# Kernel optimization log

Hardware: AMD Instinct MI355X
Metric: run time of the kernel (lower is better)

The kernel has to match this reference:

```python
import jax, jax.numpy as jnp
import numpy as np

B, N, E = 64, 128, 262144
HID, NRBF, NBLK = 128, 64, 4
RCUT = 6.0
GAMMA = 10.0 / (RCUT * RCUT)


def setup_inputs() -> dict:
    key = jax.random.key(0)
    ks = jax.random.split(key, 20)
    s_rbf = 1.0 / np.sqrt(NRBF)
    s_hid = 1.0 / np.sqrt(HID)
    return {
        "Z": jax.random.randint(ks[0], (B, N), 0, 100),
        "pos": jax.random.normal(ks[1], (B, N, 3), dtype=jnp.float32) * 3.0,
        "edge_index": jax.random.randint(ks[2], (2, E), 0, B * N),
        "embed_w": jax.random.normal(ks[3], (100, HID), dtype=jnp.float32) * 0.02,
        "edge_w1": jax.random.normal(ks[4], (NBLK, NRBF, HID), dtype=jnp.float32) * s_rbf,
        "edge_b1": jnp.zeros((NBLK, HID), dtype=jnp.float32),
        "edge_w2": jax.random.normal(ks[5], (NBLK, HID, HID), dtype=jnp.float32) * s_hid,
        "edge_b2": jnp.zeros((NBLK, HID), dtype=jnp.float32),
        "lin_in_w": jax.random.normal(ks[6], (NBLK, HID, HID), dtype=jnp.float32) * s_hid,
        "node_w1": jax.random.normal(ks[7], (NBLK, HID, HID), dtype=jnp.float32) * s_hid,
        "node_b1": jnp.zeros((NBLK, HID), dtype=jnp.float32),
        "node_w2": jax.random.normal(ks[8], (NBLK, HID, HID), dtype=jnp.float32) * s_hid,
        "node_b2": jnp.zeros((NBLK, HID), dtype=jnp.float32),
        "ln_g": jnp.ones((NBLK, HID), dtype=jnp.float32),
        "ln_b": jnp.zeros((NBLK, HID), dtype=jnp.float32),
        "ro_w1": jax.random.normal(ks[9], (HID, HID // 2), dtype=jnp.float32) * s_hid,
        "ro_b1": jnp.zeros((HID // 2,), dtype=jnp.float32),
        "ro_w2": jax.random.normal(ks[10], (HID // 2, 1), dtype=jnp.float32) * (1.0 / np.sqrt(HID // 2)),
        "ro_b2": jnp.zeros((1,), dtype=jnp.float32),
    }


def _layernorm(x, g, b, eps=1e-5):
    mu = x.mean(-1, keepdims=True)
    var = ((x - mu) ** 2).mean(-1, keepdims=True)
    return (x - mu) / jnp.sqrt(var + eps) * g + b


def reference(Z, pos, edge_index, embed_w, edge_w1, edge_b1, edge_w2, edge_b2,
              lin_in_w, node_w1, node_b1, node_w2, node_b2, ln_g, ln_b,
              ro_w1, ro_b1, ro_w2, ro_b2):
    Zf = Z.reshape(-1)               # [B*N]
    pf = pos.reshape(-1, 3)          # [B*N, 3]
    src, dst = edge_index[0], edge_index[1]

    h = embed_w[Zf]                  # [B*N, H]

    # edge RBF features
    d = jnp.linalg.norm(pf[src] - pf[dst], axis=-1)      # [E]
    d = jnp.minimum(d, RCUT)
    centers = jnp.linspace(0.0, RCUT, NRBF)
    rbf = jnp.exp(-GAMMA * (d[:, None] - centers) ** 2)  # [E, NRBF]

    for i in range(NBLK):
        # CFConv: edge filter MLP on rbf
        w = jax.nn.silu(rbf @ edge_w1[i] + edge_b1[i]) @ edge_w2[i] + edge_b2[i]  # [E,H]
        m = w * (h[src] @ lin_in_w[i])                                            # [E,H]
        agg = jnp.zeros_like(h).at[dst].add(m)                                    # scatter-add [B*N,H]
        out = jax.nn.silu(agg @ node_w1[i] + node_b1[i]) @ node_w2[i] + node_b2[i]
        h = _layernorm(h + out, ln_g[i], ln_b[i])

    # readout: SiLU -> Linear -> SiLU -> Linear
    x = jax.nn.silu(h) @ ro_w1 + ro_b1
    e_atom = (jax.nn.silu(x) @ ro_w2 + ro_b2)[:, 0]      # [B*N]
    return e_atom.reshape(B, N).sum(axis=-1)             # per-graph energies [B]
```

## Files before the change

kernel.cpp:

```cpp
#include <hip/hip_runtime.h>

#define BN 8192
#define EE 262144
#define HIDD 128
#define NRBF 64
#define NBLK 4
#define TLUT 1024
#define CAP 128
#define MROWS 32
#define RCUTF 6.0f
#define GAMMAF (10.0f / 36.0f)

typedef unsigned short u16;
typedef __attribute__((ext_vector_type(8))) short short8x;
typedef __attribute__((ext_vector_type(4))) float f32x4;

__device__ __forceinline__ float silu_f(float v) {
    return v / (1.0f + __expf(-v));
}
__device__ __forceinline__ float bf2f(u16 u) {
    return __uint_as_float(((unsigned)u) << 16);
}
__device__ __forceinline__ u16 f2bf(float f) {
    unsigned u = __float_as_uint(f);
    unsigned r = u + 0x7FFFu + ((u >> 16) & 1u);
    return (u16)(r >> 16);
}

__global__ void k_prep(const float* __restrict__ liw, const float* __restrict__ nw1,
                       const float* __restrict__ nw2, const float* __restrict__ ro1,
                       u16* __restrict__ liwT, u16* __restrict__ nw1T,
                       u16* __restrict__ nw2T, u16* __restrict__ ro1T,
                       int* __restrict__ cnt, float* __restrict__ out, int out_n) {
    int id0 = blockIdx.x * 256 + threadIdx.x;
    for (int id = id0; id < 12 * 16384; id += 65536) {
        int which = id >> 14;
        int r = id & 16383;
        int n = r >> 7, k = r & 127;
        const float* src = which < 4 ? liw : (which < 8 ? nw1 : nw2);
        u16* dst = which < 4 ? liwT : (which < 8 ? nw1T : nw2T);
        int b = which & 3;
        dst[b * 16384 + n * 128 + k] = f2bf(src[(size_t)b * 16384 + k * 128 + n]);
    }
    if (id0 < 8192) {
        cnt[id0] = 0;
        int n = id0 >> 7, k = id0 & 127;
        ro1T[n * 128 + k] = f2bf(ro1[k * 64 + n]);
        if (id0 < out_n) out[id0] = 0.0f;
    }
}

__global__ void k_edges(const int* __restrict__ ei, const float* __restrict__ pos,
                        int* __restrict__ cnt, int2* __restrict__ meta) {
    int e = blockIdx.x * 256 + threadIdx.x;
    int s = ei[e];
    int d = ei[EE + e];
    float dx = pos[s * 3 + 0] - pos[d * 3 + 0];
    float dy = pos[s * 3 + 1] - pos[d * 3 + 1];
    float dz = pos[s * 3 + 2] - pos[d * 3 + 2];
    float dist = fminf(sqrtf(dx * dx + dy * dy + dz * dz), RCUTF);
    float f = dist * ((TLUT - 1) / RCUTF);
    int i0 = (int)f;
    i0 = i0 > TLUT - 2 ? TLUT - 2 : i0;
    float fr = f - (float)i0;
    int y = (i0 << 16) | (int)(fr * 65535.0f);
    int p = atomicAdd(&cnt[d], 1);
    if (p < CAP) meta[d * CAP + p] = make_int2(s, y);
}

#define GEMM_INNER(ACC, AROW0, K)                                              \
    {                                                                          \
        float4 wv = *(float4*)&Ws[K][c0];                                      \
        float a0 = AROW0[0], a1 = AROW0[1], a2 = AROW0[2], a3 = AROW0[3];      \
        ACC[0][0] += a0 * wv.x; ACC[0][1] += a0 * wv.y;                        \
        ACC[0][2] += a0 * wv.z; ACC[0][3] += a0 * wv.w;                        \
        ACC[1][0] += a1 * wv.x; ACC[1][1] += a1 * wv.y;                        \
        ACC[1][2] += a1 * wv.z; ACC[1][3] += a1 * wv.w;                        \
        ACC[2][0] += a2 * wv.x; ACC[2][1] += a2 * wv.y;                        \
        ACC[2][2] += a2 * wv.z; ACC[2][3] += a2 * wv.w;                        \
        ACC[3][0] += a3 * wv.x; ACC[3][1] += a3 * wv.y;                        \
        ACC[3][2] += a3 * wv.z; ACC[3][3] += a3 * wv.w;                        \
    }

__global__ __launch_bounds__(256) void k_lutall(const float* __restrict__ W1a,
                                                const float* __restrict__ b1a,
                                                const float* __restrict__ W2a,
                                                const float* __restrict__ b2a,
                                                u16* __restrict__ lutall) {
    __shared__ float As[32][33];
    __shared__ float Ws[32][128];
    __shared__ float T[32][128];
    int blk = blockIdx.x >> 5;
    int r0 = (blockIdx.x & 31) * 32;
    const float* W1 = W1a + (size_t)blk * NRBF * HIDD;
    const float* b1 = b1a + blk * HIDD;
    const float* W2 = W2a + (size_t)blk * HIDD * HIDD;
    const float* b2 = b2a + blk * HIDD;
    u16* lutp = lutall + (size_t)blk * TLUT * 256;
    int tid = threadIdx.x;
    int tx = tid & 31, ty = tid >> 5;
    int c0 = tx * 4, rr = ty * 4;
    float acc[4][4] = {};
    for (int kc = 0; kc < NRBF; kc += 32) {
        int lr = tid >> 3, lc = (tid & 7) * 4;
        float dt = (r0 + lr) * (RCUTF / (TLUT - 1));
#pragma unroll
        for (int j = 0; j < 4; ++j) {
            float c = (kc + lc + j) * (RCUTF / 63.0f);
            float u = dt - c;
            As[lr][lc + j] = __expf(-GAMMAF * u * u);
        }
#pragma unroll
        for (int j = 0; j < 4; ++j) {
            int idx = tid + j * 256;
            int wr = idx >> 5, wc = (idx & 31) * 4;
            *(float4*)&Ws[wr][wc] = *(const float4*)&W1[(size_t)(kc + wr) * HIDD + wc];
        }
        __syncthreads();
#pragma unroll 8
        for (int k = 0; k < 32; ++k) {
            float ar[4] = {As[rr][k], As[rr + 1][k], As[rr + 2][k], As[rr + 3][k]};
            GEMM_INNER(acc, ar, k)
        }
        __syncthreads();
    }
#pragma unroll
    for (int i = 0; i < 4; ++i)
#pragma unroll
        for (int j = 0; j < 4; ++j)
            T[rr + i][c0 + j] = silu_f(acc[i][j] + b1[c0 + j]);
    float acc2[4][4] = {};
    __syncthreads();
    for (int kc = 0; kc < HIDD; kc += 32) {
#pragma unroll
        for (int j = 0; j < 4; ++j) {
            int idx = tid + j * 256;
            int wr = idx >> 5, wc = (idx & 31) * 4;
            *(float4*)&Ws[wr][wc] = *(const float4*)&W2[(size_t)(kc + wr) * HIDD + wc];
        }
        __syncthreads();
#pragma unroll 8
        for (int k = 0; k < 32; ++k) {
            float ar[4] = {T[rr][kc + k], T[rr + 1][kc + k], T[rr + 2][kc + k],
                           T[rr + 3][kc + k]};
            GEMM_INNER(acc2, ar, k)
        }
        __syncthreads();
    }
#pragma unroll
    for (int i = 0; i < 4; ++i) {
        int t = r0 + rr + i;
        ushort2 a01, a23;
        a01.x = f2bf(acc2[i][0] + b2[c0 + 0]);
        a01.y = f2bf(acc2[i][1] + b2[c0 + 1]);
        a23.x = f2bf(acc2[i][2] + b2[c0 + 2]);
        a23.y = f2bf(acc2[i][3] + b2[c0 + 3]);
        u16* pa = lutp + ((size_t)t * 64 + (c0 >> 1)) * 4;
        *(ushort2*)(pa + 0) = a01;
        *(ushort2*)(pa + 4) = a23;
        if (t > 0) {
            u16* pb = lutp + ((size_t)(t - 1) * 64 + (c0 >> 1)) * 4;
            *(ushort2*)(pb + 2) = a01;
            *(ushort2*)(pb + 6) = a23;
        }
    }
}

__global__ __launch_bounds__(256, 4) void k_agg(const int* __restrict__ cnt,
                                                const int2* __restrict__ meta,
                                                const u16* __restrict__ lutp,
                                                const u16* __restrict__ xin,
                                                u16* __restrict__ aggb) {
    int dst = blockIdx.x * 4 + (threadIdx.x >> 6);
    int lane = threadIdx.x & 63;
    int n = cnt[dst];
    n = n > CAP ? CAP : n;
    const int2* mp = meta + (size_t)dst * CAP;
    int nm1 = n > 0 ? n - 1 : 0;
    int ja = lane < nm1 ? lane : nm1;
    int jb = 64 + lane < nm1 ? 64 + lane : nm1;
    int2 md1 = mp[ja];
    int2 md2 = mp[jb];
    float ax = 0.0f, ay = 0.0f;
#pragma unroll 4
    for (int t = 0; t < n; ++t) {
        int mx = __shfl(t < 64 ? md1.x : md2.x, t & 63);
        int my = __shfl(t < 64 ? md1.y : md2.y, t & 63);
        int i0 = my >> 16;
        float fr = (my & 0xffff) * (1.0f / 65535.0f);
        ushort4 lv = *(const ushort4*)&lutp[(((size_t)i0 << 6) + lane) << 2];
        ushort2 xv = *(const ushort2*)&xin[((size_t)mx << 7) + 2 * lane];
        float w0x = bf2f(lv.x), w0y = bf2f(lv.y);
        float wx = fmaf(fr, bf2f(lv.z) - w0x, w0x);
        float wy = fmaf(fr, bf2f(lv.w) - w0y, w0y);
        ax = fmaf(wx, bf2f(xv.x), ax);
        ay = fmaf(wy, bf2f(xv.y), ay);
    }
    ushort2 o;
    o.x = f2bf(ax);
    o.y = f2bf(ay);
    *(ushort2*)&aggb[((size_t)dst << 7) + 2 * lane] = o;
}

__device__ __forceinline__ void stage_wt(u16 Wt[][136], const u16* __restrict__ src,
                                         int rows) {
    int tid = threadIdx.x;
    int chunks = rows * 16;
    for (int idx = tid; idx < chunks; idx += 256) {
        int r = idx >> 4, c = (idx & 15) * 8;
        *(float4*)&Wt[r][c] = *(const float4*)&src[r * 128 + c];
    }
}

__device__ __forceinline__ void gemm32(const u16 A[][136], const u16 B[][136],
                                       int n0, f32x4 acc[2][2]) {
    int l = threadIdx.x & 63;
    int m = l & 15, q = (l >> 4) * 8;
#pragma unroll
    for (int kc = 0; kc < 128; kc += 32) {
        short8x a0 = *(const short8x*)&A[m][kc + q];
        short8x a1 = *(const short8x*)&A[16 + m][kc + q];
        short8x b0 = *(const short8x*)&B[n0 + m][kc + q];
        short8x b1 = *(const short8x*)&B[n0 + 16 + m][kc + q];
        acc[0][0] = __builtin_amdgcn_mfma_f32_16x16x32_bf16(a0, b0, acc[0][0], 0, 0, 0);
        acc[0][1] = __builtin_amdgcn_mfma_f32_16x16x32_bf16(a0, b1, acc[0][1], 0, 0, 0);
        acc[1][0] = __builtin_amdgcn_mfma_f32_16x16x32_bf16(a1, b0, acc[1][0], 0, 0, 0);
        acc[1][1] = __builtin_amdgcn_mfma_f32_16x16x32_bf16(a1, b1, acc[1][1], 0, 0, 0);
    }
}

__global__ __launch_bounds__(256, 2) void k_embedx(const int* __restrict__ Z,
                                                   const float* __restrict__ ew,
                                                   const u16* __restrict__ liwT0,
                                                   float* __restrict__ h,
                                                   u16* __restrict__ xb) {
    __shared__ u16 Wt[128][136];
    __shared__ u16 Ab[MROWS][136];
    int tid = threadIdx.x;
    int r0 = blockIdx.x * MROWS;
    {
        int row = tid >> 3, c16 = (tid & 7) * 16;
        int z = Z[r0 + row];
        const float* er = ew + (size_t)z * HIDD + c16;
        float* hr = h + (size_t)(r0 + row) * HIDD + c16;
#pragma unroll
        for (int j = 0; j < 4; ++j) {
            float4 v = *(const float4*)(er + 4 * j);
            *(float4*)(hr + 4 * j) = v;
            ushort4 a;
            a.x = f2bf(v.x); a.y = f2bf(v.y); a.z = f2bf(v.z); a.w = f2bf(v.w);
            *(ushort4*)&Ab[row][c16 + 4 * j] = a;
        }
    }
    stage_wt(Wt, liwT0, 128);
    __syncthreads();
    int w = tid >> 6, l = tid & 63;
    int m = l & 15, q = l >> 4;
    f32x4 acc[2][2] = {{{0, 0, 0, 0}, {0, 0, 0, 0}}, {{0, 0, 0, 0}, {0, 0, 0, 0}}};
    gemm32(Ab, Wt, w * 32, acc);
    int c = w * 32 + m;
#pragma unroll
    for (int half = 0; half < 2; ++half)
#pragma unroll
        for (int r = 0; r < 4; ++r) {
            int row = half * 16 + q * 4 + r;
            u16* xr = xb + (size_t)(r0 + row) * HIDD;
            xr[c] = f2bf(acc[half][0][r]);
            xr[c + 16] = f2bf(acc[half][1][r]);
        }
}

__global__ __launch_bounds__(256, 2) void k_mlp(
    const u16* __restrict__ aggb, float* __restrict__ h,
    const u16* __restrict__ w1t, const float* __restrict__ b1,
    const u16* __restrict__ w2t, const float* __restrict__ b2,
    const float* __restrict__ g, const float* __restrict__ bb,
    const u16* __restrict__ w3t, u16* __restrict__ xout, int last,
    const float* __restrict__ rb1, const float* __restrict__ rw2,
    const float* __restrict__ rb2, float* __restrict__ out) {
    __shared__ u16 Wt[128][136];
    __shared__ u16 Ab[MROWS][136];
    __shared__ u16 Tb[MROWS][136];
    __shared__ float Hf[MROWS][132];
    __shared__ float red[4];
    int tid = threadIdx.x;
    int w = tid >> 6, l = tid & 63;
    int m = l & 15, q = l >> 4;
    int r0 = blockIdx.x * MROWS;

    {
        int row = tid >> 3, c8 = (tid & 7) * 16;
        const u16* ar = aggb + ((size_t)(r0 + row) << 7) + c8;
        *(float4*)&Ab[row][c8] = *(const float4*)ar;
        *(float4*)&Ab[row][c8 + 8] = *(const float4*)(ar + 8);
    }
    stage_wt(Wt, w1t, 128);
    __syncthreads();

    {
        f32x4 acc[2][2] = {{{0, 0, 0, 0}, {0, 0, 0, 0}}, {{0, 0, 0, 0}, {0, 0, 0, 0}}};
        gemm32(Ab, Wt, w * 32, acc);
        int c = w * 32 + m;
        float bv0 = b1[c], bv1 = b1[c + 16];
        __syncthreads();
#pragma unroll
        for (int half = 0; half < 2; ++half)
#pragma unroll
            for (int r = 0; r < 4; ++r) {
                int row = half * 16 + q * 4 + r;
                Tb[row][c] = f2bf(silu_f(acc[half][0][r] + bv0));
                Tb[row][c + 16] = f2bf(silu_f(acc[half][1][r] + bv1));
            }
    }
    stage_wt(Wt, w2t, 128);
    __syncthreads();

    {
        f32x4 acc[2][2] = {{{0, 0, 0, 0}, {0, 0, 0, 0}}, {{0, 0, 0, 0}, {0, 0, 0, 0}}};
        gemm32(Tb, Wt, w * 32, acc);
        int c = w * 32 + m;
        float bv0 = b2[c], bv1 = b2[c + 16];
        __syncthreads();
#pragma unroll
        for (int half = 0; half < 2; ++half)
#pragma unroll
            for (int r = 0; r < 4; ++r) {
                int row = half * 16 + q * 4 + r;
                const float* hr = h + (size_t)(r0 + row) * HIDD;
                Hf[row][c] = acc[half][0][r] + bv0 + hr[c];
                Hf[row][c + 16] = acc[half][1][r] + bv1 + hr[c + 16];
            }
    }
    stage_wt(Wt, w3t, last ? 64 : 128);
    __syncthreads();

    {
        float gx = g[2 * l], gy = g[2 * l + 1];
        float bx = bb[2 * l], by = bb[2 * l + 1];
#pragma unroll
        for (int rr = 0; rr < 8; ++rr) {
            int row = w * 8 + rr;
            float2 v = *(float2*)&Hf[row][2 * l];
            float s = v.x + v.y;
#pragma unroll
            for (int mm = 32; mm; mm >>= 1) s += __shfl_xor(s, mm);
            float mu = s * (1.0f / 128.0f);
            float dx = v.x - mu, dy = v.y - mu;
            float qq = dx * dx + dy * dy;
#pragma unroll
            for (int mm = 32; mm; mm >>= 1) qq += __shfl_xor(qq, mm);
            float rstd = rsqrtf(qq * (1.0f / 128.0f) + 1e-5f);
            float ox = dx * rstd * gx + bx;
            float oy = dy * rstd * gy + by;
            if (!last) {
                float2 o;
                o.x = ox;
                o.y = oy;
                *(float2*)&h[(size_t)(r0 + row) * HIDD + 2 * l] = o;
            }
            ushort2 a;
            a.x = f2bf(last ? silu_f(ox) : ox);
            a.y = f2bf(last ? silu_f(oy) : oy);
            *(ushort2*)&Ab[row][2 * l] = a;
        }
    }
    __syncthreads();

    if (!last) {
        f32x4 acc[2][2] = {{{0, 0, 0, 0}, {0, 0, 0, 0}}, {{0, 0, 0, 0}, {0, 0, 0, 0}}};
        gemm32(Ab, Wt, w * 32, acc);
        int c = w * 32 + m;
#pragma unroll
        for (int half = 0; half < 2; ++half)
#pragma unroll
            for (int r = 0; r < 4; ++r) {
                int row = half * 16 + q * 4 + r;
                u16* xr = xout + (size_t)(r0 + row) * HIDD;
                xr[c] = f2bf(acc[half][0][r]);
                xr[c + 16] = f2bf(acc[half][1][r]);
            }
    } else {
        f32x4 a0 = {0, 0, 0, 0}, a1 = {0, 0, 0, 0};
        int n0 = w * 16;
        int qq8 = q * 8;
#pragma unroll
        for (int kc = 0; kc < 128; kc += 32) {
            short8x av0 = *(const short8x*)&Ab[m][kc + qq8];
            short8x av1 = *(const short8x*)&Ab[16 + m][kc + qq8];
            short8x bv = *(const short8x*)&Wt[n0 + m][kc + qq8];
            a0 = __builtin_amdgcn_mfma_f32_16x16x32_bf16(av0, bv, a0, 0, 0, 0);
            a1 = __builtin_amdgcn_mfma_f32_16x16x32_bf16(av1, bv, a1, 0, 0, 0);
        }
        int c = n0 + m;
        float bv = rb1[c], wv = rw2[c];
        float tsum = 0.0f;
#pragma unroll
        for (int r = 0; r < 4; ++r) {
            tsum += silu_f(a0[r] + bv) * wv;
            tsum += silu_f(a1[r] + bv) * wv;
        }
#pragma unroll
        for (int mm = 32; mm; mm >>= 1) tsum += __shfl_xor(tsum, mm);
        if (l == 0) red[w] = tsum;
        __syncthreads();
        if (tid == 0) {
            float tot = red[0] + red[1] + red[2] + red[3] + (float)MROWS * rb2[0];
            atomicAdd(&out[r0 >> 7], tot);
        }
    }
}

extern "C" void kernel_launch(void* const* d_in, const int* in_sizes, int n_in,
                              void* d_out, int out_size, void* d_ws, size_t ws_size,
                              hipStream_t stream) {
    const int*   Z   = (const int*)d_in[0];
    const float* pos = (const float*)d_in[1];
    const int*   ei  = (const int*)d_in[2];
    const float* ew  = (const float*)d_in[3];
    const float* ew1 = (const float*)d_in[4];
    const float* eb1 = (const float*)d_in[5];
    const float* ew2 = (const float*)d_in[6];
    const float* eb2 = (const float*)d_in[7];
    const float* liw = (const float*)d_in[8];
    const float* nw1 = (const float*)d_in[9];
    const float* nb1 = (const float*)d_in[10];
    const float* nw2 = (const float*)d_in[11];
    const float* nb2 = (const float*)d_in[12];
    const float* lng = (const float*)d_in[13];
    const float* lnb = (const float*)d_in[14];
    const float* rw1 = (const float*)d_in[15];
    const float* rb1 = (const float*)d_in[16];
    const float* rw2 = (const float*)d_in[17];
    const float* rb2 = (const float*)d_in[18];
    float* out = (float*)d_out;

    float* h      = (float*)d_ws;
    u16*   xb0    = (u16*)(h + (size_t)BN * HIDD);
    u16*   xb1    = xb0 + (size_t)BN * HIDD;
    u16*   aggb   = xb1 + (size_t)BN * HIDD;
    u16*   lutall = aggb + (size_t)BN * HIDD;
    u16*   liwT   = lutall + (size_t)NBLK * TLUT * 256;
    u16*   nw1T   = liwT + (size_t)NBLK * HIDD * HIDD;
    u16*   nw2T   = nw1T + (size_t)NBLK * HIDD * HIDD;
    u16*   ro1T   = nw2T + (size_t)NBLK * HIDD * HIDD;
    int*   cnt    = (int*)(ro1T + 64 * HIDD);
    int2*  meta   = (int2*)(cnt + BN);

    k_prep<<<256, 256, 0, stream>>>(liw, nw1, nw2, rw1, liwT, nw1T, nw2T, ro1T,
                                    cnt, out, out_size);
    k_edges<<<EE / 256, 256, 0, stream>>>(ei, pos, cnt, meta);
    k_lutall<<<NBLK * (TLUT / 32), 256, 0, stream>>>(ew1, eb1, ew2, eb2, lutall);
    k_embedx<<<BN / MROWS, 256, 0, stream>>>(Z, ew, liwT, h, xb0);

    u16* xbuf[2] = {xb0, xb1};
    for (int i = 0; i < NBLK; ++i) {
        int last = (i == NBLK - 1);
        k_agg<<<BN / 4, 256, 0, stream>>>(cnt, meta, lutall + (size_t)i * TLUT * 256,
                                          xbuf[i & 1], aggb);
        k_mlp<<<BN / MROWS, 256, 0, stream>>>(
            aggb, h,
            nw1T + (size_t)i * HIDD * HIDD, nb1 + i * HIDD,
            nw2T + (size_t)i * HIDD * HIDD, nb2 + i * HIDD,
            lng + i * HIDD, lnb + i * HIDD,
            last ? ro1T : liwT + (size_t)(i + 1) * HIDD * HIDD,
            last ? (u16*)nullptr : xbuf[(i + 1) & 1],
            last, rb1, rw2, rb2, out);
    }
}
```

Before: 255.9 us.

## Fuse setup kernels and switch edge-filter LUT to nearest-neighbor lookup

Four setup kernels (weight transpose, edge binning, LUT build, embedding projection) are merged into one launch whose blocks are partitioned by role, and the counter is cleared with a memset. The edge-filter lookup table doubles its resolution but drops linear interpolation, so each edge does a single nearest-entry read. Edge metadata is packed into one int (LUT index plus source node), which halves the meta traffic in the aggregation loop. This trades interpolation accuracy for fewer loads and less arithmetic per edge, and the fused setup relies on its roles not depending on each other. The embedding blocks each rebuild the transposed first-layer weight in shared memory.

```diff
diff --git a/kernel.cpp b/kernel.cpp
--- a/kernel.cpp
+++ b/kernel.cpp
@@ -5,9 +5,10 @@
 #define HIDD 128
 #define NRBF 64
 #define NBLK 4
-#define TLUT 1024
+#define TLUT 2048
 #define CAP 128
 #define MROWS 32
+#define MR 16
 #define RCUTF 6.0f
 #define GAMMAF (10.0f / 36.0f)
 
@@ -25,181 +26,6 @@
     unsigned u = __float_as_uint(f);
     unsigned r = u + 0x7FFFu + ((u >> 16) & 1u);
     return (u16)(r >> 16);
-}
-
-__global__ void k_prep(const float* __restrict__ liw, const float* __restrict__ nw1,
-                       const float* __restrict__ nw2, const float* __restrict__ ro1,
-                       u16* __restrict__ liwT, u16* __restrict__ nw1T,
-                       u16* __restrict__ nw2T, u16* __restrict__ ro1T,
-                       int* __restrict__ cnt, float* __restrict__ out, int out_n) {
-    int id0 = blockIdx.x * 256 + threadIdx.x;
-    for (int id = id0; id < 12 * 16384; id += 65536) {
-        int which = id >> 14;
-        int r = id & 16383;
-        int n = r >> 7, k = r & 127;
-        const float* src = which < 4 ? liw : (which < 8 ? nw1 : nw2);
-        u16* dst = which < 4 ? liwT : (which < 8 ? nw1T : nw2T);
-        int b = which & 3;
-        dst[b * 16384 + n * 128 + k] = f2bf(src[(size_t)b * 16384 + k * 128 + n]);
-    }
-    if (id0 < 8192) {
-        cnt[id0] = 0;
-        int n = id0 >> 7, k = id0 & 127;
-        ro1T[n * 128 + k] = f2bf(ro1[k * 64 + n]);
-        if (id0 < out_n) out[id0] = 0.0f;
-    }
-}
-
-__global__ void k_edges(const int* __restrict__ ei, const float* __restrict__ pos,
-                        int* __restrict__ cnt, int2* __restrict__ meta) {
-    int e = blockIdx.x * 256 + threadIdx.x;
-    int s = ei[e];
-    int d = ei[EE + e];
-    float dx = pos[s * 3 + 0] - pos[d * 3 + 0];
-    float dy = pos[s * 3 + 1] - pos[d * 3 + 1];
-    float dz = pos[s * 3 + 2] - pos[d * 3 + 2];
-    float dist = fminf(sqrtf(dx * dx + dy * dy + dz * dz), RCUTF);
-    float f = dist * ((TLUT - 1) / RCUTF);
-    int i0 = (int)f;
-    i0 = i0 > TLUT - 2 ? TLUT - 2 : i0;
-    float fr = f - (float)i0;
-    int y = (i0 << 16) | (int)(fr * 65535.0f);
-    int p = atomicAdd(&cnt[d], 1);
-    if (p < CAP) meta[d * CAP + p] = make_int2(s, y);
-}
-
-#define GEMM_INNER(ACC, AROW0, K)                                              \
-    {                                                                          \
-        float4 wv = *(float4*)&Ws[K][c0];                                      \
-        float a0 = AROW0[0], a1 = AROW0[1], a2 = AROW0[2], a3 = AROW0[3];      \
-        ACC[0][0] += a0 * wv.x; ACC[0][1] += a0 * wv.y;                        \
-        ACC[0][2] += a0 * wv.z; ACC[0][3] += a0 * wv.w;                        \
-        ACC[1][0] += a1 * wv.x; ACC[1][1] += a1 * wv.y;                        \
-        ACC[1][2] += a1 * wv.z; ACC[1][3] += a1 * wv.w;                        \
-        ACC[2][0] += a2 * wv.x; ACC[2][1] += a2 * wv.y;                        \
-        ACC[2][2] += a2 * wv.z; ACC[2][3] += a2 * wv.w;                        \
-        ACC[3][0] += a3 * wv.x; ACC[3][1] += a3 * wv.y;                        \
-        ACC[3][2] += a3 * wv.z; ACC[3][3] += a3 * wv.w;                        \
-    }
-
-__global__ __launch_bounds__(256) void k_lutall(const float* __restrict__ W1a,
-                                                const float* __restrict__ b1a,
-                                                const float* __restrict__ W2a,
-                                                const float* __restrict__ b2a,
-                                                u16* __restrict__ lutall) {
-    __shared__ float As[32][33];
-    __shared__ float Ws[32][128];
-    __shared__ float T[32][128];
-    int blk = blockIdx.x >> 5;
-    int r0 = (blockIdx.x & 31) * 32;
-    const float* W1 = W1a + (size_t)blk * NRBF * HIDD;
-    const float* b1 = b1a + blk * HIDD;
-    const float* W2 = W2a + (size_t)blk * HIDD * HIDD;
-    const float* b2 = b2a + blk * HIDD;
-    u16* lutp = lutall + (size_t)blk * TLUT * 256;
-    int tid = threadIdx.x;
-    int tx = tid & 31, ty = tid >> 5;
-    int c0 = tx * 4, rr = ty * 4;
-    float acc[4][4] = {};
-    for (int kc = 0; kc < NRBF; kc += 32) {
-        int lr = tid >> 3, lc = (tid & 7) * 4;
-        float dt = (r0 + lr) * (RCUTF / (TLUT - 1));
-#pragma unroll
-        for (int j = 0; j < 4; ++j) {
-            float c = (kc + lc + j) * (RCUTF / 63.0f);
-            float u = dt - c;
-            As[lr][lc + j] = __expf(-GAMMAF * u * u);
-        }
-#pragma unroll
-        for (int j = 0; j < 4; ++j) {
-            int idx = tid + j * 256;
-            int wr = idx >> 5, wc = (idx & 31) * 4;
-            *(float4*)&Ws[wr][wc] = *(const float4*)&W1[(size_t)(kc + wr) * HIDD + wc];
-        }
-        __syncthreads();
-#pragma unroll 8
-        for (int k = 0; k < 32; ++k) {
-            float ar[4] = {As[rr][k], As[rr + 1][k], As[rr + 2][k], As[rr + 3][k]};
-            GEMM_INNER(acc, ar, k)
-        }
-        __syncthreads();
-    }
-#pragma unroll
-    for (int i = 0; i < 4; ++i)
-#pragma unroll
-        for (int j = 0; j < 4; ++j)
-            T[rr + i][c0 + j] = silu_f(acc[i][j] + b1[c0 + j]);
-    float acc2[4][4] = {};
-    __syncthreads();
-    for (int kc = 0; kc < HIDD; kc += 32) {
-#pragma unroll
-        for (int j = 0; j < 4; ++j) {
-            int idx = tid + j * 256;
-            int wr = idx >> 5, wc = (idx & 31) * 4;
-            *(float4*)&Ws[wr][wc] = *(const float4*)&W2[(size_t)(kc + wr) * HIDD + wc];
-        }
-        __syncthreads();
-#pragma unroll 8
-        for (int k = 0; k < 32; ++k) {
-            float ar[4] = {T[rr][kc + k], T[rr + 1][kc + k], T[rr + 2][kc + k],
-                           T[rr + 3][kc + k]};
-            GEMM_INNER(acc2, ar, k)
-        }
-        __syncthreads();
-    }
-#pragma unroll
-    for (int i = 0; i < 4; ++i) {
-        int t = r0 + rr + i;
-        ushort2 a01, a23;
-        a01.x = f2bf(acc2[i][0] + b2[c0 + 0]);
-        a01.y = f2bf(acc2[i][1] + b2[c0 + 1]);
-        a23.x = f2bf(acc2[i][2] + b2[c0 + 2]);
-        a23.y = f2bf(acc2[i][3] + b2[c0 + 3]);
-        u16* pa = lutp + ((size_t)t * 64 + (c0 >> 1)) * 4;
-        *(ushort2*)(pa + 0) = a01;
-        *(ushort2*)(pa + 4) = a23;
-        if (t > 0) {
-            u16* pb = lutp + ((size_t)(t - 1) * 64 + (c0 >> 1)) * 4;
-            *(ushort2*)(pb + 2) = a01;
-            *(ushort2*)(pb + 6) = a23;
-        }
-    }
-}
-
-__global__ __launch_bounds__(256, 4) void k_agg(const int* __restrict__ cnt,
-                                                const int2* __restrict__ meta,
-                                                const u16* __restrict__ lutp,
-                                                const u16* __restrict__ xin,
-                                                u16* __restrict__ aggb) {
-    int dst = blockIdx.x * 4 + (threadIdx.x >> 6);
-    int lane = threadIdx.x & 63;
-    int n = cnt[dst];
-    n = n > CAP ? CAP : n;
-    const int2* mp = meta + (size_t)dst * CAP;
-    int nm1 = n > 0 ? n - 1 : 0;
-    int ja = lane < nm1 ? lane : nm1;
-    int jb = 64 + lane < nm1 ? 64 + lane : nm1;
-    int2 md1 = mp[ja];
-    int2 md2 = mp[jb];
-    float ax = 0.0f, ay = 0.0f;
-#pragma unroll 4
-    for (int t = 0; t < n; ++t) {
-        int mx = __shfl(t < 64 ? md1.x : md2.x, t & 63);
-        int my = __shfl(t < 64 ? md1.y : md2.y, t & 63);
-        int i0 = my >> 16;
-        float fr = (my & 0xffff) * (1.0f / 65535.0f);
-        ushort4 lv = *(const ushort4*)&lutp[(((size_t)i0 << 6) + lane) << 2];
-        ushort2 xv = *(const ushort2*)&xin[((size_t)mx << 7) + 2 * lane];
-        float w0x = bf2f(lv.x), w0y = bf2f(lv.y);
-        float wx = fmaf(fr, bf2f(lv.z) - w0x, w0x);
-        float wy = fmaf(fr, bf2f(lv.w) - w0y, w0y);
-        ax = fmaf(wx, bf2f(xv.x), ax);
-        ay = fmaf(wy, bf2f(xv.y), ay);
-    }
-    ushort2 o;
-    o.x = f2bf(ax);
-    o.y = f2bf(ay);
-    *(ushort2*)&aggb[((size_t)dst << 7) + 2 * lane] = o;
 }
 
 __device__ __forceinline__ void stage_wt(u16 Wt[][136], const u16* __restrict__ src,
@@ -208,20 +34,34 @@
     int chunks = rows * 16;
     for (int idx = tid; idx < chunks; idx += 256) {
         int r = idx >> 4, c = (idx & 15) * 8;
-        *(float4*)&Wt[r][c] = *(const float4*)&src[r * 128 + c];
+        *(float4*)&Wt[r][c] = *(const float4*)&src[r * HIDD + c];
+    }
+}
+
+__device__ __forceinline__ void gemm16(const u16 A[][136], const u16 B[][136],
+                                       int n0, f32x4& a0, f32x4& a1) {
+    int l = threadIdx.x & 63;
+    int m = l & 15, q8 = (l >> 4) * 8;
+#pragma unroll
+    for (int kc = 0; kc < 128; kc += 32) {
+        short8x av = *(const short8x*)&A[m][kc + q8];
+        short8x b0 = *(const short8x*)&B[n0 + m][kc + q8];
+        short8x b1 = *(const short8x*)&B[n0 + 16 + m][kc + q8];
+        a0 = __builtin_amdgcn_mfma_f32_16x16x32_bf16(av, b0, a0, 0, 0, 0);
+        a1 = __builtin_amdgcn_mfma_f32_16x16x32_bf16(av, b1, a1, 0, 0, 0);
     }
 }
 
 __device__ __forceinline__ void gemm32(const u16 A[][136], const u16 B[][136],
                                        int n0, f32x4 acc[2][2]) {
     int l = threadIdx.x & 63;
-    int m = l & 15, q = (l >> 4) * 8;
+    int m = l & 15, q8 = (l >> 4) * 8;
 #pragma unroll
     for (int kc = 0; kc < 128; kc += 32) {
-        short8x a0 = *(const short8x*)&A[m][kc + q];
-        short8x a1 = *(const short8x*)&A[16 + m][kc + q];
-        short8x b0 = *(const short8x*)&B[n0 + m][kc + q];
-        short8x b1 = *(const short8x*)&B[n0 + 16 + m][kc + q];
+        short8x a0 = *(const short8x*)&A[m][kc + q8];
+        short8x a1 = *(const short8x*)&A[16 + m][kc + q8];
+        short8x b0 = *(const short8x*)&B[n0 + m][kc + q8];
+        short8x b1 = *(const short8x*)&B[n0 + 16 + m][kc + q8];
         acc[0][0] = __builtin_amdgcn_mfma_f32_16x16x32_bf16(a0, b0, acc[0][0], 0, 0, 0);
         acc[0][1] = __builtin_amdgcn_mfma_f32_16x16x32_bf16(a0, b1, acc[0][1], 0, 0, 0);
         acc[1][0] = __builtin_amdgcn_mfma_f32_16x16x32_bf16(a1, b0, acc[1][0], 0, 0, 0);
@@ -229,45 +69,205 @@
     }
 }
 
-__global__ __launch_bounds__(256, 2) void k_embedx(const int* __restrict__ Z,
-                                                   const float* __restrict__ ew,
-                                                   const u16* __restrict__ liwT0,
-                                                   float* __restrict__ h,
-                                                   u16* __restrict__ xb) {
-    __shared__ u16 Wt[128][136];
-    __shared__ u16 Ab[MROWS][136];
-    int tid = threadIdx.x;
-    int r0 = blockIdx.x * MROWS;
-    {
-        int row = tid >> 3, c16 = (tid & 7) * 16;
-        int z = Z[r0 + row];
-        const float* er = ew + (size_t)z * HIDD + c16;
-        float* hr = h + (size_t)(r0 + row) * HIDD + c16;
-#pragma unroll
-        for (int j = 0; j < 4; ++j) {
-            float4 v = *(const float4*)(er + 4 * j);
-            *(float4*)(hr + 4 * j) = v;
-            ushort4 a;
-            a.x = f2bf(v.x); a.y = f2bf(v.y); a.z = f2bf(v.z); a.w = f2bf(v.w);
-            *(ushort4*)&Ab[row][c16 + 4 * j] = a;
-        }
-    }
-    stage_wt(Wt, liwT0, 128);
-    __syncthreads();
-    int w = tid >> 6, l = tid & 63;
-    int m = l & 15, q = l >> 4;
-    f32x4 acc[2][2] = {{{0, 0, 0, 0}, {0, 0, 0, 0}}, {{0, 0, 0, 0}, {0, 0, 0, 0}}};
-    gemm32(Ab, Wt, w * 32, acc);
-    int c = w * 32 + m;
-#pragma unroll
-    for (int half = 0; half < 2; ++half)
+__global__ __launch_bounds__(256) void k_setup(
+    const int* __restrict__ Z, const float* __restrict__ pos,
+    const int* __restrict__ ei, const float* __restrict__ ew,
+    const float* __restrict__ ew1, const float* __restrict__ eb1,
+    const float* __restrict__ ew2, const float* __restrict__ eb2,
+    const float* __restrict__ liw, const float* __restrict__ nw1,
+    const float* __restrict__ nw2, const float* __restrict__ ro1,
+    int* __restrict__ cnt, int* __restrict__ meta, u16* __restrict__ lutall,
+    float* __restrict__ h, u16* __restrict__ xb0,
+    u16* __restrict__ liwT, u16* __restrict__ nw1T, u16* __restrict__ nw2T,
+    u16* __restrict__ ro1T, float* __restrict__ out, int out_n) {
+    __shared__ union {
+        struct { u16 Wt[128][136]; u16 Ab[MR][136]; } ex;
+        struct { float As[32 * 33]; float Ws[32 * 128]; float T2[32 * 128]; } lu;
+    } S;
+    int tid = threadIdx.x, blk = blockIdx.x;
+
+    if (blk < 1024) {
+        int e = blk * 256 + tid;
+        int s = ei[e];
+        int d = ei[EE + e];
+        float dx = pos[s * 3 + 0] - pos[d * 3 + 0];
+        float dy = pos[s * 3 + 1] - pos[d * 3 + 1];
+        float dz = pos[s * 3 + 2] - pos[d * 3 + 2];
+        float dist = fminf(sqrtf(dx * dx + dy * dy + dz * dz), RCUTF);
+        int i0 = (int)(dist * ((TLUT - 1) / RCUTF) + 0.5f);
+        i0 = i0 > TLUT - 1 ? TLUT - 1 : i0;
+        int p = atomicAdd(&cnt[d], 1);
+        if (p < CAP) meta[(size_t)d * CAP + p] = (i0 << 13) | s;
+    } else if (blk < 1280) {
+        int lb = blk - 1024;
+        int net = lb >> 6;
+        int r0l = (lb & 63) * 32;
+        const float* W1 = ew1 + (size_t)net * NRBF * HIDD;
+        const float* b1 = eb1 + net * HIDD;
+        const float* W2 = ew2 + (size_t)net * HIDD * HIDD;
+        const float* b2 = eb2 + net * HIDD;
+        u16* lutp = lutall + (size_t)net * TLUT * HIDD;
+        int tx = tid & 31, ty = tid >> 5;
+        int c0 = tx * 4, rr = ty * 4;
+        float acc[4][4] = {};
+        for (int kc = 0; kc < NRBF; kc += 32) {
+            int lr = tid >> 3, lc = (tid & 7) * 4;
+            float dt = (r0l + lr) * (RCUTF / (TLUT - 1));
+#pragma unroll
+            for (int j = 0; j < 4; ++j) {
+                float c = (kc + lc + j) * (RCUTF / 63.0f);
+                float u = dt - c;
+                S.lu.As[lr * 33 + lc + j] = __expf(-GAMMAF * u * u);
+            }
+#pragma unroll
+            for (int j = 0; j < 4; ++j) {
+                int idx = tid + j * 256;
+                int wr = idx >> 5, wc = (idx & 31) * 4;
+                *(float4*)&S.lu.Ws[wr * 128 + wc] =
+                    *(const float4*)&W1[(size_t)(kc + wr) * HIDD + wc];
+            }
+            __syncthreads();
+#pragma unroll 8
+            for (int k = 0; k < 32; ++k) {
+                float4 wv = *(float4*)&S.lu.Ws[k * 128 + c0];
+                float a0 = S.lu.As[(rr + 0) * 33 + k];
+                float a1 = S.lu.As[(rr + 1) * 33 + k];
+                float a2 = S.lu.As[(rr + 2) * 33 + k];
+                float a3 = S.lu.As[(rr + 3) * 33 + k];
+                acc[0][0] += a0 * wv.x; acc[0][1] += a0 * wv.y; acc[0][2] += a0 * wv.z; acc[0][3] += a0 * wv.w;
+                acc[1][0] += a1 * wv.x; acc[1][1] += a1 * wv.y; acc[1][2] += a1 * wv.z; acc[1][3] += a1 * wv.w;
+                acc[2][0] += a2 * wv.x; acc[2][1] += a2 * wv.y; acc[2][2] += a2 * wv.z; acc[2][3] += a2 * wv.w;
+                acc[3][0] += a3 * wv.x; acc[3][1] += a3 * wv.y; acc[3][2] += a3 * wv.z; acc[3][3] += a3 * wv.w;
+            }
+            __syncthreads();
+        }
+#pragma unroll
+        for (int i = 0; i < 4; ++i)
+#pragma unroll
+            for (int j = 0; j < 4; ++j)
+                S.lu.T2[(rr + i) * 128 + c0 + j] = silu_f(acc[i][j] + b1[c0 + j]);
+        float acc2[4][4] = {};
+        __syncthreads();
+        for (int kc = 0; kc < HIDD; kc += 32) {
+#pragma unroll
+            for (int j = 0; j < 4; ++j) {
+                int idx = tid + j * 256;
+                int wr = idx >> 5, wc = (idx & 31) * 4;
+                *(float4*)&S.lu.Ws[wr * 128 + wc] =
+                    *(const float4*)&W2[(size_t)(kc + wr) * HIDD + wc];
+            }
+            __syncthreads();
+#pragma unroll 8
+            for (int k = 0; k < 32; ++k) {
+                float4 wv = *(float4*)&S.lu.Ws[k * 128 + c0];
+                float a0 = S.lu.T2[(rr + 0) * 128 + kc + k];
+                float a1 = S.lu.T2[(rr + 1) * 128 + kc + k];
+                float a2 = S.lu.T2[(rr + 2) * 128 + kc + k];
+                float a3 = S.lu.T2[(rr + 3) * 128 + kc + k];
+                acc2[0][0] += a0 * wv.x; acc2[0][1] += a0 * wv.y; acc2[0][2] += a0 * wv.z; acc2[0][3] += a0 * wv.w;
+                acc2[1][0] += a1 * wv.x; acc2[1][1] += a1 * wv.y; acc2[1][2] += a1 * wv.z; acc2[1][3] += a1 * wv.w;
+                acc2[2][0] += a2 * wv.x; acc2[2][1] += a2 * wv.y; acc2[2][2] += a2 * wv.z; acc2[2][3] += a2 * wv.w;
+                acc2[3][0] += a3 * wv.x; acc2[3][1] += a3 * wv.y; acc2[3][2] += a3 * wv.z; acc2[3][3] += a3 * wv.w;
+            }
+            __syncthreads();
+        }
+#pragma unroll
+        for (int i = 0; i < 4; ++i) {
+            int t = r0l + rr + i;
+            ushort4 o;
+            o.x = f2bf(acc2[i][0] + b2[c0 + 0]);
+            o.y = f2bf(acc2[i][1] + b2[c0 + 1]);
+            o.z = f2bf(acc2[i][2] + b2[c0 + 2]);
+            o.w = f2bf(acc2[i][3] + b2[c0 + 3]);
+            *(ushort4*)&lutp[(size_t)t * HIDD + c0] = o;
+        }
+    } else if (blk < 1792) {
+        int r0 = (blk - 1280) * MR;
+        for (int idx = tid; idx < 16384; idx += 256) {
+            int n = idx & 127, k = idx >> 7;
+            S.ex.Wt[n][k] = f2bf(liw[(size_t)k * 128 + n]);
+        }
+        {
+            int row = tid >> 4, c8 = (tid & 15) * 8;
+            int z = Z[r0 + row];
+            const float* er = ew + (size_t)z * HIDD + c8;
+            float* hr = h + (size_t)(r0 + row) * HIDD + c8;
+            float4 v0 = *(const float4*)er;
+            float4 v1 = *(const float4*)(er + 4);
+            *(float4*)hr = v0;
+            *(float4*)(hr + 4) = v1;
+            ushort4 a0, a1;
+            a0.x = f2bf(v0.x); a0.y = f2bf(v0.y); a0.z = f2bf(v0.z); a0.w = f2bf(v0.w);
+            a1.x = f2bf(v1.x); a1.y = f2bf(v1.y); a1.z = f2bf(v1.z); a1.w = f2bf(v1.w);
+            *(ushort4*)&S.ex.Ab[row][c8] = a0;
+            *(ushort4*)&S.ex.Ab[row][c8 + 4] = a1;
+        }
+        __syncthreads();
+        int w = tid >> 6, l = tid & 63;
+        int m = l & 15, q4 = l >> 4;
+        f32x4 a0 = {0, 0, 0, 0}, a1 = {0, 0, 0, 0};
+        gemm16(S.ex.Ab, S.ex.Wt, w * 32, a0, a1);
+        int c = w * 32 + m;
 #pragma unroll
         for (int r = 0; r < 4; ++r) {
-            int row = half * 16 + q * 4 + r;
-            u16* xr = xb + (size_t)(r0 + row) * HIDD;
-            xr[c] = f2bf(acc[half][0][r]);
-            xr[c + 16] = f2bf(acc[half][1][r]);
-        }
+            int row = q4 * 4 + r;
+            u16* xr = xb0 + (size_t)(r0 + row) * HIDD;
+            xr[c] = f2bf(a0[r]);
+            xr[c + 16] = f2bf(a1[r]);
+        }
+    } else {
+        for (int id = (blk - 1792) * 256 + tid; id < 188416; id += 128 * 256) {
+            if (id < 180224) {
+                int which = id >> 14;
+                int r = id & 16383;
+                int n = r >> 7, k = r & 127;
+                const float* src;
+                u16* dst;
+                if (which < 3) { src = liw + (size_t)(which + 1) * 16384;
+                                 dst = liwT + (size_t)(which + 1) * 16384; }
+                else if (which < 7) { src = nw1 + (size_t)(which - 3) * 16384;
+                                      dst = nw1T + (size_t)(which - 3) * 16384; }
+                else { src = nw2 + (size_t)(which - 7) * 16384;
+                       dst = nw2T + (size_t)(which - 7) * 16384; }
+                dst[n * 128 + k] = f2bf(src[(size_t)k * 128 + n]);
+            } else {
+                int rid = id - 180224;
+                int n = rid >> 7, k = rid & 127;
+                ro1T[n * 128 + k] = f2bf(ro1[(size_t)k * 64 + n]);
+            }
+        }
+        if (blk == 1792 && tid < out_n) out[tid] = 0.0f;
+    }
+}
+
+__global__ __launch_bounds__(256, 4) void k_agg(const int* __restrict__ cnt,
+                                                const int* __restrict__ meta,
+                                                const u16* __restrict__ lut,
+                                                const u16* __restrict__ xin,
+                                                u16* __restrict__ aggb) {
+    int dst = blockIdx.x * 4 + (threadIdx.x >> 6);
+    int l = threadIdx.x & 63;
+    int n = cnt[dst];
+    n = n > CAP ? CAP : n;
+    const int* mp = meta + (size_t)dst * CAP;
+    int nm1 = n > 0 ? n - 1 : 0;
+    int mA = mp[l < nm1 ? l : nm1];
+    int mB = mp[64 + l < nm1 ? 64 + l : nm1];
+    float ax = 0.0f, ay = 0.0f;
+#pragma unroll 4
+    for (int t = 0; t < n; ++t) {
+        int md = __shfl(t < 64 ? mA : mB, t & 63);
+        int s = md & 8191;
+        int i0 = md >> 13;
+        ushort2 lv = *(const ushort2*)&lut[((size_t)i0 << 7) + 2 * l];
+        ushort2 xv = *(const ushort2*)&xin[((size_t)s << 7) + 2 * l];
+        ax = fmaf(bf2f(lv.x), bf2f(xv.x), ax);
+        ay = fmaf(bf2f(lv.y), bf2f(xv.y), ay);
+    }
+    ushort2 o;
+    o.x = f2bf(ax);
+    o.y = f2bf(ay);
+    *(ushort2*)&aggb[((size_t)dst << 7) + 2 * l] = o;
 }
 
 __global__ __launch_bounds__(256, 2) void k_mlp(
@@ -285,7 +285,7 @@
     __shared__ float red[4];
     int tid = threadIdx.x;
     int w = tid >> 6, l = tid & 63;
-    int m = l & 15, q = l >> 4;
+    int m = l & 15, q4 = l >> 4, q8 = q4 * 8;
     int r0 = blockIdx.x * MROWS;
 
     {
@@ -307,7 +307,7 @@
         for (int half = 0; half < 2; ++half)
 #pragma unroll
             for (int r = 0; r < 4; ++r) {
-                int row = half * 16 + q * 4 + r;
+                int row = half * 16 + q4 * 4 + r;
                 Tb[row][c] = f2bf(silu_f(acc[half][0][r] + bv0));
                 Tb[row][c + 16] = f2bf(silu_f(acc[half][1][r] + bv1));
             }
@@ -325,7 +325,7 @@
         for (int half = 0; half < 2; ++half)
 #pragma unroll
             for (int r = 0; r < 4; ++r) {
-                int row = half * 16 + q * 4 + r;
+                int row = half * 16 + q4 * 4 + r;
                 const float* hr = h + (size_t)(r0 + row) * HIDD;
                 Hf[row][c] = acc[half][0][r] + bv0 + hr[c];
                 Hf[row][c + 16] = acc[half][1][r] + bv1 + hr[c + 16];
@@ -374,7 +374,7 @@
         for (int half = 0; half < 2; ++half)
 #pragma unroll
             for (int r = 0; r < 4; ++r) {
-                int row = half * 16 + q * 4 + r;
+                int row = half * 16 + q4 * 4 + r;
                 u16* xr = xout + (size_t)(r0 + row) * HIDD;
                 xr[c] = f2bf(acc[half][0][r]);
                 xr[c + 16] = f2bf(acc[half][1][r]);
@@ -382,12 +382,11 @@
     } else {
         f32x4 a0 = {0, 0, 0, 0}, a1 = {0, 0, 0, 0};
         int n0 = w * 16;
-        int qq8 = q * 8;
 #pragma unroll
         for (int kc = 0; kc < 128; kc += 32) {
-            short8x av0 = *(const short8x*)&Ab[m][kc + qq8];
-            short8x av1 = *(const short8x*)&Ab[16 + m][kc + qq8];
-            short8x bv = *(const short8x*)&Wt[n0 + m][kc + qq8];
+            short8x av0 = *(const short8x*)&Ab[m][kc + q8];
+            short8x av1 = *(const short8x*)&Ab[16 + m][kc + q8];
+            short8x bv = *(const short8x*)&Wt[n0 + m][kc + q8];
             a0 = __builtin_amdgcn_mfma_f32_16x16x32_bf16(av0, bv, a0, 0, 0, 0);
             a1 = __builtin_amdgcn_mfma_f32_16x16x32_bf16(av1, bv, a1, 0, 0, 0);
         }
@@ -439,23 +438,24 @@
     u16*   xb1    = xb0 + (size_t)BN * HIDD;
     u16*   aggb   = xb1 + (size_t)BN * HIDD;
     u16*   lutall = aggb + (size_t)BN * HIDD;
-    u16*   liwT   = lutall + (size_t)NBLK * TLUT * 256;
+    u16*   liwT   = lutall + (size_t)NBLK * TLUT * HIDD;
     u16*   nw1T   = liwT + (size_t)NBLK * HIDD * HIDD;
     u16*   nw2T   = nw1T + (size_t)NBLK * HIDD * HIDD;
     u16*   ro1T   = nw2T + (size_t)NBLK * HIDD * HIDD;
     int*   cnt    = (int*)(ro1T + 64 * HIDD);
-    int2*  meta   = (int2*)(cnt + BN);
-
-    k_prep<<<256, 256, 0, stream>>>(liw, nw1, nw2, rw1, liwT, nw1T, nw2T, ro1T,
-                                    cnt, out, out_size);
-    k_edges<<<EE / 256, 256, 0, stream>>>(ei, pos, cnt, meta);
-    k_lutall<<<NBLK * (TLUT / 32), 256, 0, stream>>>(ew1, eb1, ew2, eb2, lutall);
-    k_embedx<<<BN / MROWS, 256, 0, stream>>>(Z, ew, liwT, h, xb0);
+    int*   meta   = (int*)(cnt + BN);
+
+    (void)hipMemsetAsync(cnt, 0, BN * sizeof(int), stream);
+    k_setup<<<1920, 256, 0, stream>>>(Z, pos, ei, ew, ew1, eb1, ew2, eb2,
+                                      liw, nw1, nw2, rw1,
+                                      cnt, meta, lutall, h, xb0,
+                                      liwT, nw1T, nw2T, ro1T, out, out_size);
 
     u16* xbuf[2] = {xb0, xb1};
     for (int i = 0; i < NBLK; ++i) {
         int last = (i == NBLK - 1);
-        k_agg<<<BN / 4, 256, 0, stream>>>(cnt, meta, lutall + (size_t)i * TLUT * 256,
+        k_agg<<<BN / 4, 256, 0, stream>>>(cnt, meta,
+                                          lutall + (size_t)i * TLUT * HIDD,
                                           xbuf[i & 1], aggb);
         k_mlp<<<BN / MROWS, 256, 0, stream>>>(
             aggb, h,
```

Result: slower. 289.3 us (+13.0%).
